# Performance work log

Measured on AMD Instinct MI355X. Metric: run time of the kernel, lower is better.

## Reference

```python
import jax, jax.numpy as jnp
import numpy as np

B, T, C, L = 1024, 256, 128, 64
NEG = -1e30  # finite stand-in for -inf (safe gradients)
EPS = 1e-7   # keras.backend.epsilon()


def setup_inputs() -> dict:
    key = jax.random.key(0)
    k1, k2 = jax.random.split(key)
    # y_pred is a softmax output (probabilities), as keras ctc_batch_cost expects
    logits = jax.random.normal(k1, (B, T, C), dtype=jnp.float32)
    y_pred = jax.nn.softmax(logits, axis=-1)
    # labels in [0, C-2]; class C-1 is the CTC blank (keras convention)
    y_true = jax.random.randint(k2, (B, L), 0, C - 1, dtype=jnp.int64)
    return {"y_true": y_true, "y_pred": y_pred}


def ctc_loss(y_true, y_pred):
    """Negative log-likelihood CTC loss per sample, shape [B, 1].
    Matches keras.backend.ctc_batch_cost with full input/label lengths,
    blank index = num_classes - 1, log(y_pred + eps)."""
    Bb, Tt, Cc = y_pred.shape
    Ll = y_true.shape[1]
    blank = Cc - 1
    S = 2 * Ll + 1  # extended label: blank, l1, blank, l2, ..., blank

    logp = jnp.log(y_pred + EPS)  # [B, T, C]

    ext = jnp.full((Bb, S), blank, dtype=y_true.dtype).at[:, 1::2].set(y_true)  # [B, S]
    # per-(t, s) log-prob of the extended symbol: lp[b, t, s] = logp[b, t, ext[b, s]]
    lp = jnp.take_along_axis(logp, ext[:, None, :], axis=2)  # [B, T, S]

    # skip transition s-2 -> s allowed iff ext[s] != blank and ext[s] != ext[s-2]
    ext_m2 = jnp.concatenate(
        [jnp.full((Bb, 2), blank, dtype=ext.dtype), ext[:, :-2]], axis=1)
    can_skip = (ext != blank) & (ext != ext_m2)  # [B, S]

    def shift1(a):
        return jnp.concatenate(
            [jnp.full((Bb, 1), NEG, dtype=a.dtype), a[:, :-1]], axis=1)

    # alpha init at t=0: only s=0 (blank) and s=1 (first label) reachable
    alpha0 = (jnp.full((Bb, S), NEG, dtype=lp.dtype)
              .at[:, 0].set(lp[:, 0, 0])
              .at[:, 1].set(lp[:, 0, 1]))

    def step(alpha, lp_t):
        a1 = shift1(alpha)
        a2 = jnp.where(can_skip, shift1(shift1(alpha)), NEG)
        new = jax.nn.logsumexp(jnp.stack([alpha, a1, a2], axis=0), axis=0) + lp_t
        return new, None

    lp_tbs = jnp.swapaxes(lp, 0, 1)  # [T, B, S]
    alpha, _ = jax.lax.scan(step, alpha0, lp_tbs[1:])

    log_lik = jnp.logaddexp(alpha[:, S - 1], alpha[:, S - 2])  # end on last blank or last label
    return -log_lik[:, None]  # [B, 1], matching ctc_batch_cost output shape


def reference(y_true, y_pred):
    return ctc_loss(y_true, y_pred)
```

## Files before the change

### kernel.cpp

```cpp
#include <hip/hip_runtime.h>
#include <math.h>


#define Bn 1024
#define Tn 256
#define Cn 128
#define Ln 64
#define BLANK 127
#define U 8
#define NG (Tn / U)
#define EPS128 (1e-7f * 128.0f)
#define LN2 0.69314718055994530942f

template <int CTRL>
__device__ __forceinline__ float dpp_mov(float x) {
    return __int_as_float(__builtin_amdgcn_update_dpp(
        0, __float_as_int(x), CTRL, 0xF, 0xF, true));
}

__global__ __launch_bounds__(64)
void ctc_prob_kernel(const int* __restrict__ y_true,
                     const float* __restrict__ y_pred,
                     float* __restrict__ out) {
    const int b = blockIdx.x;
    const int i = threadIdx.x;
    const bool lane0 = (i == 0);

    const int* lab = y_true + b * Ln;
    const int li   = lab[i];
    const int prev = lab[(i == 0) ? 0 : (i - 1)];
    const bool skip = (i == 0) || (li != prev);

    const float* base = y_pred + (size_t)b * (Tn * Cn);
    const float* pl = base + li;
    const float* pb = base + BLANK;

    float rlA[U], rbA[U], rlB[U], rbB[U], ql[U], qb[U];
    float A0 = 0.0f, Aod = 0.0f, Aev = 0.0f;
    int Esum = 0;

    auto issue = [&](int g, float* rl, float* rb) {
        const float* l  = pl + (size_t)g * (U * Cn);
        const float* bl = pb + (size_t)g * (U * Cn);
#pragma unroll
        for (int j = 0; j < U; ++j) { rl[j] = l[j * Cn]; rb[j] = bl[j * Cn]; }
    };
    auto convert = [&](const float* rl, const float* rb) {
#pragma unroll
        for (int j = 0; j < U; ++j) {
            ql[j] = fmaf(rl[j], 128.0f, EPS128);
            qb[j] = fmaf(rb[j], 128.0f, EPS128);
        }
    };
    auto steps = [&](bool first) {
#pragma unroll
        for (int j = 0; j < U; ++j) {
            if (first && j == 0) {
                A0  = qb[0];
                Aod = lane0 ? ql[0] : 0.0f;
                Aev = 0.0f;
                continue;
            }
            const float odL = dpp_mov<0x138>(Aod);
            const float evS = dpp_mov<0x138>(Aev);
            const float evL = lane0 ? A0 : evS;
            const float sk  = skip ? odL : 0.0f;
            const float nev = (Aev + Aod) * qb[j];
            const float nod = (Aod + evL + sk) * ql[j];
            A0 *= qb[j];
            Aod = nod;
            Aev = nev;
        }
    };
    auto renorm = [&]() {
        float m = fmaxf(A0, fmaxf(Aod, Aev));
        m = fmaxf(m, dpp_mov<0x111>(m));
        m = fmaxf(m, dpp_mov<0x112>(m));
        m = fmaxf(m, dpp_mov<0x114>(m));
        m = fmaxf(m, dpp_mov<0x118>(m));
        m = fmaxf(m, dpp_mov<0x142>(m));
        m = fmaxf(m, dpp_mov<0x143>(m));
        const unsigned ub = (unsigned)__builtin_amdgcn_readlane(__float_as_int(m), 63);
        const int ebits = (int)(ub >> 23);
        const float sc = __int_as_float((254 - ebits) << 23);
        Esum += ebits - 127;
        A0 *= sc; Aod *= sc; Aev *= sc;
    };

    issue(0, rlA, rbA);
    issue(1, rlB, rbB);
    convert(rlA, rbA);
    issue(2, rlA, rbA);
    steps(true);
    renorm();

    for (int g = 1; g < NG - 1; g += 2) {
        convert(rlB, rbB);
        if (g + 2 < NG) issue(g + 2, rlB, rbB);
        steps(false);
        renorm();
        convert(rlA, rbA);
        if (g + 3 < NG) issue(g + 3, rlA, rbA);
        steps(false);
        renorm();
    }

    convert(rlB, rbB);
    steps(false);

    if (i == 63) {
        const float s  = Aod + Aev;
#if __has_builtin(__builtin_amdgcn_logf)
        const float l2 = __builtin_amdgcn_logf(s) + (float)(Esum - 7 * Tn);
#else
        const float l2 = log2f(s) + (float)(Esum - 7 * Tn);
#endif
        out[b] = -l2 * LN2;
    }
}

extern "C" void kernel_launch(void* const* d_in, const int* in_sizes, int n_in,
                              void* d_out, int out_size, void* d_ws, size_t ws_size,
                              hipStream_t stream) {
    const int*   y_true = (const int*)d_in[0];
    const float* y_pred = (const float*)d_in[1];
    float*       out    = (float*)d_out;
    hipLaunchKernelGGL(ctc_prob_kernel, dim3(Bn), dim3(64), 0, stream,
                       y_true, y_pred, out);
}
```

Baseline: 193.8 us.

## Stage probability tiles through LDS with coalesced float4 loads

Replaces the per-lane strided gathers of the label and blank columns with fully coalesced float4 loads of whole 8-timestep chunks. The chunks are double-buffered in shared memory, and each lane reads its label and blank probabilities from LDS. The alpha recurrence is also reorganised into E/O/X state variables, dropping the lane-0 special case and using a float skip factor inside an fma. This aims to cut uncoalesced global memory traffic, but it reads every class column and adds LDS writes and reads without explicit barriers, relying on single-wavefront execution.

```diff
diff --git a/kernel.cpp b/kernel.cpp
--- a/kernel.cpp
+++ b/kernel.cpp
@@ -8,114 +8,110 @@
 #define Ln 64
 #define BLANK 127
 #define U 8
-#define NG (Tn / U)
+#define NC (Tn / U)
 #define EPS128 (1e-7f * 128.0f)
 #define LN2 0.69314718055994530942f
 
 template <int CTRL>
-__device__ __forceinline__ float dpp_mov(float x) {
+__device__ __forceinline__ float dpp_movf(float x) {
     return __int_as_float(__builtin_amdgcn_update_dpp(
         0, __float_as_int(x), CTRL, 0xF, 0xF, true));
 }
+__device__ __forceinline__ int dpp_shr1_i(int x) {
+    return __builtin_amdgcn_update_dpp(0, x, 0x138, 0xF, 0xF, true);
+}
 
 __global__ __launch_bounds__(64)
-void ctc_prob_kernel(const int* __restrict__ y_true,
-                     const float* __restrict__ y_pred,
-                     float* __restrict__ out) {
+void ctc_lds_kernel(const int* __restrict__ y_true,
+                    const float* __restrict__ y_pred,
+                    float* __restrict__ out) {
     const int b = blockIdx.x;
     const int i = threadIdx.x;
-    const bool lane0 = (i == 0);
 
-    const int* lab = y_true + b * Ln;
-    const int li   = lab[i];
-    const int prev = lab[(i == 0) ? 0 : (i - 1)];
-    const bool skip = (i == 0) || (li != prev);
+    __shared__ __align__(16) float prob[2][U * Cn];
 
-    const float* base = y_pred + (size_t)b * (Tn * Cn);
-    const float* pl = base + li;
-    const float* pb = base + BLANK;
+    const int li = y_true[b * Ln + i];
+    const int ll = dpp_shr1_i(li);
+    const float skf = (li != ll) ? 1.0f : 0.0f;
 
-    float rlA[U], rbA[U], rlB[U], rbB[U], ql[U], qb[U];
-    float A0 = 0.0f, Aod = 0.0f, Aev = 0.0f;
+    const float4* gsrc = (const float4*)(y_pred + (size_t)b * (Tn * Cn));
+    float4 ra[4], rb[4];
+
+    auto gload = [&](int c, float4* r) {
+        const float4* p = gsrc + c * (U * Cn / 4) + i;
+#pragma unroll
+        for (int k = 0; k < 4; ++k) r[k] = p[k * 64];
+    };
+    auto lwrite = [&](int buf, const float4* r) {
+        float4* d = ((float4*)prob[buf]) + i;
+#pragma unroll
+        for (int k = 0; k < 4; ++k) d[k * 64] = r[k];
+    };
+
+    float E = 0.f, O = 0.f, X = 0.f;
     int Esum = 0;
 
-    auto issue = [&](int g, float* rl, float* rb) {
-        const float* l  = pl + (size_t)g * (U * Cn);
-        const float* bl = pb + (size_t)g * (U * Cn);
-#pragma unroll
-        for (int j = 0; j < U; ++j) { rl[j] = l[j * Cn]; rb[j] = bl[j * Cn]; }
-    };
-    auto convert = [&](const float* rl, const float* rb) {
+    auto steps = [&](const float* pr, bool first) {
 #pragma unroll
         for (int j = 0; j < U; ++j) {
-            ql[j] = fmaf(rl[j], 128.0f, EPS128);
-            qb[j] = fmaf(rb[j], 128.0f, EPS128);
-        }
-    };
-    auto steps = [&](bool first) {
-#pragma unroll
-        for (int j = 0; j < U; ++j) {
+            const float* row = pr + j * Cn;
+            const float ql = fmaf(row[li],    128.0f, EPS128);
+            const float qb = fmaf(row[BLANK], 128.0f, EPS128);
             if (first && j == 0) {
-                A0  = qb[0];
-                Aod = lane0 ? ql[0] : 0.0f;
-                Aev = 0.0f;
+                E = (i == 0) ? qb : 0.f;
+                O = (i == 0) ? ql : 0.f;
+                X = 0.f;
                 continue;
             }
-            const float odL = dpp_mov<0x138>(Aod);
-            const float evS = dpp_mov<0x138>(Aev);
-            const float evL = lane0 ? A0 : evS;
-            const float sk  = skip ? odL : 0.0f;
-            const float nev = (Aev + Aod) * qb[j];
-            const float nod = (Aod + evL + sk) * ql[j];
-            A0 *= qb[j];
-            Aod = nod;
-            Aev = nev;
+            const float Ol = dpp_movf<0x138>(O);
+            const float t1 = O + E;
+            const float nO = fmaf(skf, Ol, t1) * ql;
+            const float nE = (E + Ol) * qb;
+            const float nX = (X + O) * qb;
+            E = nE; O = nO; X = nX;
         }
     };
     auto renorm = [&]() {
-        float m = fmaxf(A0, fmaxf(Aod, Aev));
-        m = fmaxf(m, dpp_mov<0x111>(m));
-        m = fmaxf(m, dpp_mov<0x112>(m));
-        m = fmaxf(m, dpp_mov<0x114>(m));
-        m = fmaxf(m, dpp_mov<0x118>(m));
-        m = fmaxf(m, dpp_mov<0x142>(m));
-        m = fmaxf(m, dpp_mov<0x143>(m));
-        const unsigned ub = (unsigned)__builtin_amdgcn_readlane(__float_as_int(m), 63);
-        const int ebits = (int)(ub >> 23);
-        const float sc = __int_as_float((254 - ebits) << 23);
-        Esum += ebits - 127;
-        A0 *= sc; Aod *= sc; Aev *= sc;
+        float m = fmaxf(E, O);
+        if (i == 63) m = fmaxf(m, X);
+        m = fmaxf(m, dpp_movf<0x111>(m));
+        m = fmaxf(m, dpp_movf<0x112>(m));
+        m = fmaxf(m, dpp_movf<0x114>(m));
+        m = fmaxf(m, dpp_movf<0x118>(m));
+        m = fmaxf(m, dpp_movf<0x142>(m));
+        m = fmaxf(m, dpp_movf<0x143>(m));
+        const unsigned ub =
+            (unsigned)__builtin_amdgcn_readlane(__float_as_int(m), 63);
+        const int eb = (int)(ub >> 23);
+        const float sc = __int_as_float((unsigned)(254 - eb) << 23);
+        Esum += eb - 127;
+        E *= sc; O *= sc; X *= sc;
     };
 
-    issue(0, rlA, rbA);
-    issue(1, rlB, rbB);
-    convert(rlA, rbA);
-    issue(2, rlA, rbA);
-    steps(true);
-    renorm();
+    gload(0, ra);
+    gload(1, rb);
+    lwrite(0, ra);
+    gload(2, ra);
 
-    for (int g = 1; g < NG - 1; g += 2) {
-        convert(rlB, rbB);
-        if (g + 2 < NG) issue(g + 2, rlB, rbB);
-        steps(false);
+    for (int c = 0; c < NC; c += 2) {
+        lwrite(1, rb);
+        if (c + 3 < NC) gload(c + 3, rb);
+        steps(prob[0], c == 0);
         renorm();
-        convert(rlA, rbA);
-        if (g + 3 < NG) issue(g + 3, rlA, rbA);
-        steps(false);
-        renorm();
+        lwrite(0, ra);
+        if (c + 4 < NC) gload(c + 4, ra);
+        steps(prob[1], false);
+        if (c + 2 < NC) renorm();
     }
 
-    convert(rlB, rbB);
-    steps(false);
-
     if (i == 63) {
-        const float s  = Aod + Aev;
+        const float s = O + X;
 #if __has_builtin(__builtin_amdgcn_logf)
-        const float l2 = __builtin_amdgcn_logf(s) + (float)(Esum - 7 * Tn);
+        const float l2 = __builtin_amdgcn_logf(s);
 #else
-        const float l2 = log2f(s) + (float)(Esum - 7 * Tn);
+        const float l2 = log2f(s);
 #endif
-        out[b] = -l2 * LN2;
+        out[b] = -(l2 + (float)(Esum - 7 * Tn)) * LN2;
     }
 }
 
@@ -125,6 +121,6 @@
     const int*   y_true = (const int*)d_in[0];
     const float* y_pred = (const float*)d_in[1];
     float*       out    = (float*)d_out;
-    hipLaunchKernelGGL(ctc_prob_kernel, dim3(Bn), dim3(64), 0, stream,
+    hipLaunchKernelGGL(ctc_lds_kernel, dim3(Bn), dim3(64), 0, stream,
                        y_true, y_pred, out);
 }
```

Result: slower. 207.3 us (+7.0%).
